# Kernel optimization log

Hardware: AMD Instinct MI355X
Metric: run time of the kernel (lower is better)

Reference implementation:

```python
import jax, jax.numpy as jnp
import numpy as np

L = 3            # max degree for L_in = L_edge = L_out = (0, 3)
B = 1024         # batch (number of edges)
C_IN = 256
C_OUT = 256
NUM_ORDERS = (L + 1) ** 2  # 16


def _build_structure(L):
    """Rebuild the coo_CG sparse structure: nonzeros sorted by (M_out, l1, l2),
    using the CG selection rule m1 + m2 = m for valid triangle triples."""
    triples = {}
    for l1 in range(L + 1):
        for l2 in range(L + 1):
            for l in range(abs(l1 - l2), min(L, l1 + l2) + 1):
                key = (l, l1, l2)
                if key not in triples:
                    triples[key] = len(triples)
    M1, M2, seg1, lind_g, seg2 = [], [], [], [], []
    g = 0
    for l in range(L + 1):
        for m in range(-l, l + 1):
            M = l * l + l + m  # flat order index of (l, m)
            for (lo, l1, l2) in sorted(triples.keys()):
                if lo != l:
                    continue
                cnt = 0
                for m1 in range(-l1, l1 + 1):
                    m2 = m - m1
                    if -l2 <= m2 <= l2:
                        M1.append(l1 * l1 + l1 + m1)
                        M2.append(l2 * l2 + l2 + m2)
                        seg1.append(g)
                        cnt += 1
                if cnt > 0:
                    lind_g.append(triples[(lo, l1, l2)])
                    seg2.append(M)
                    g += 1
    return (np.asarray(M1, np.int32), np.asarray(M2, np.int32),
            np.asarray(seg1, np.int32), np.asarray(lind_g, np.int32),
            np.asarray(seg2, np.int32), len(triples), g)


def setup_inputs() -> dict:
    key = jax.random.key(0)
    k1, k2, k3, k4 = jax.random.split(key, 4)
    M1, M2, seg1, l_ind, seg2, n_w, n_g = _build_structure(L)
    # expected: 478 nnz, 156 groups, 34 weights
    x = jax.random.normal(k1, (B, NUM_ORDERS, C_IN), jnp.float32)
    sh = jax.random.normal(k2, (B, NUM_ORDERS), jnp.float32)
    fan = np.sqrt(2.0 / (C_IN + C_OUT)).astype(np.float32)
    weight = jax.random.normal(k3, (n_w, C_IN, C_OUT), jnp.float32) * fan
    CG_vals = jax.random.normal(k4, (M1.shape[0],), jnp.float32) * 0.3
    return {
        'x': x, 'sh': sh, 'weight': weight, 'CG_vals': CG_vals,
        'M1': jnp.asarray(M1), 'M2': jnp.asarray(M2), 'seg1': jnp.asarray(seg1),
        'l_ind': jnp.asarray(l_ind), 'seg2': jnp.asarray(seg2),
        'num_orders_out': NUM_ORDERS,
    }


def reference(x, sh, weight, CG_vals, M1, M2, seg1, l_ind, seg2, num_orders_out):
    # x: (B, Mi, Ci); sh: (B, Me); weight: (num_weights, Ci, Co)
    Bn = x.shape[0]
    G = l_ind.shape[0]
    Ci = x.shape[-1]
    Co = weight.shape[-1]
    feat = x[:, M1, :]                                      # (B, nnz, Ci) gather on orders
    sh_g = sh[:, M2]                                        # (B, nnz)
    inter = (CG_vals[None, :] * sh_g)[..., None] * feat     # (B, nnz, Ci)
    inter = jnp.zeros((Bn, G, Ci), x.dtype).at[:, seg1, :].add(inter)   # segment over (M,l1,l2)
    w = weight[l_ind]                                       # (G, Ci, Co)
    ret = jnp.einsum('bgi,gio->bgo', inter, w)              # per-group matmul
    out = jnp.zeros((Bn, num_orders_out, Co), x.dtype).at[:, seg2, :].add(ret)  # segment over M
    return out
```

## Files before the change

### kernel.cpp

```cpp
#include <hip/hip_runtime.h>
#include <stdint.h>

#define B_SZ 1024
#define NO   16
#define CI   256
#define CO   256
#define BK   64
#define BM   32
#define LDA  72
#define MAXG 12
#define MAXE 48
#define WP   76

typedef unsigned short u16;
typedef __attribute__((ext_vector_type(8))) short short8;
typedef __attribute__((ext_vector_type(4))) float f32x4;
typedef __attribute__((ext_vector_type(4))) unsigned short u16x4;
typedef __attribute__((ext_vector_type(8))) unsigned short u16x8;

__device__ __forceinline__ u16 f2bf(float f) {
  union { float f; uint32_t u; } v; v.f = f;
  uint32_t u = v.u;
  return (u16)((u + 0x7FFFu + ((u >> 16) & 1u)) >> 16);
}
__device__ __forceinline__ float bf2f(u16 h) {
  union { float f; uint32_t u; } v; v.u = ((uint32_t)h) << 16; return v.f;
}

__device__ __forceinline__ f32x4 mfma_16x16x32_bf16(short8 a, short8 b, f32x4 c) {
  asm volatile("v_mfma_f32_16x16x32_bf16 %0, %1, %2, %0" : "+v"(c) : "v"(a), "v"(b));
  return c;
}

extern "C" __global__ void xconv_kernel(const float* __restrict__ x,
                                        u16* __restrict__ xbf, int n8) {
  int t = blockIdx.x * 256 + threadIdx.x;
  if (t >= n8) return;
  const float* s = x + (size_t)t * 8;
  float4 a = ((const float4*)s)[0];
  float4 b = ((const float4*)s)[1];
  u16x8 pk;
  pk[0] = f2bf(a.x); pk[1] = f2bf(a.y); pk[2] = f2bf(a.z); pk[3] = f2bf(a.w);
  pk[4] = f2bf(b.x); pk[5] = f2bf(b.y); pk[6] = f2bf(b.z); pk[7] = f2bf(b.w);
  *(u16x8*)(xbf + (size_t)t * 8) = pk;
}

extern "C" __global__ void wconv_kernel(const float* __restrict__ w,
                                        u16* __restrict__ wbf) {
  __shared__ u16 t_lds[64 * WP];
  const int tid = threadIdx.x;
  const int bid = blockIdx.x;
  const int wi = bid >> 4;
  const int i0 = ((bid >> 2) & 3) * 64;
  const int o0 = (bid & 3) * 64;
  const float* src = w + (size_t)wi * (CI * CO);
  u16* dst = wbf + (size_t)wi * (CI * CO);
#pragma unroll
  for (int p = 0; p < 4; ++p) {
    int idx = p * 256 + tid;
    int i = idx >> 4, oq = (idx & 15) * 4;
    float4 v = *(const float4*)(src + (size_t)(i0 + i) * CO + o0 + oq);
    t_lds[(oq + 0) * WP + i] = f2bf(v.x);
    t_lds[(oq + 1) * WP + i] = f2bf(v.y);
    t_lds[(oq + 2) * WP + i] = f2bf(v.z);
    t_lds[(oq + 3) * WP + i] = f2bf(v.w);
  }
  __syncthreads();
#pragma unroll
  for (int p = 0; p < 4; ++p) {
    int idx = p * 256 + tid;
    int o = idx >> 4, iq = (idx & 15) * 4;
    u16x4 v;
    v[0] = t_lds[o * WP + iq + 0]; v[1] = t_lds[o * WP + iq + 1];
    v[2] = t_lds[o * WP + iq + 2]; v[3] = t_lds[o * WP + iq + 3];
    *(u16x4*)(dst + (size_t)(o0 + o) * CI + i0 + iq) = v;
  }
}

extern "C" __global__ void __launch_bounds__(256, 4)
so3_main(const u16* __restrict__ xbf,
         const float* __restrict__ sh,
         const float* __restrict__ CG,
         const u16* __restrict__ wbf,
         const int* __restrict__ M1,
         const int* __restrict__ M2,
         const int* __restrict__ seg1,
         const int* __restrict__ lind,
         const int* __restrict__ seg2,
         float* __restrict__ out,
         int G, int nnz) {
  __shared__ u16 As[BM * LDA];
  __shared__ u16 Bs[128 * LDA];
  __shared__ float coefs[MAXE][BM];
  __shared__ int s_meta[4];
  __shared__ int s_estart[MAXG], s_eend[MAXG], s_wind[MAXG], s_m1[MAXE];

  const int tid = threadIdx.x;
  const int bid = blockIdx.x;
  const int b0  = (bid & 31) * BM;
  const int M   = (bid >> 5) & 15;
  const int co0 = (bid >> 9) * 128;

  if (tid == 0) { s_meta[0] = 1 << 30; s_meta[1] = 0; s_meta[2] = 1 << 30; s_meta[3] = 0; }
  if (tid < MAXG) { s_estart[tid] = 1 << 30; s_eend[tid] = 0; }
  __syncthreads();
  for (int g = tid; g < G; g += 256)
    if (seg2[g] == M) { atomicMin(&s_meta[0], g); atomicMax(&s_meta[1], g + 1); }
  __syncthreads();
  const int gstart = s_meta[0];
  const int ng = s_meta[1] - gstart;
  for (int e = tid; e < nnz; e += 256) {
    int g = seg1[e] - gstart;
    if (g >= 0 && g < ng) {
      atomicMin(&s_meta[2], e); atomicMax(&s_meta[3], e + 1);
      atomicMin(&s_estart[g], e); atomicMax(&s_eend[g], e + 1);
    }
  }
  __syncthreads();
  const int e0 = s_meta[2];
  const int ne = s_meta[3] - e0;
  for (int i = tid; i < ng; i += 256) s_wind[i] = lind[gstart + i];
  for (int i = tid; i < ne; i += 256) s_m1[i] = M1[e0 + i];
  for (int idx = tid; idx < ne * BM; idx += 256) {
    int el = idx / BM, r = idx & (BM - 1);
    int e = e0 + el;
    coefs[el][r] = CG[e] * sh[(size_t)(b0 + r) * NO + M2[e]];
  }
  __syncthreads();

  const int lane = tid & 63;
  const int wn = tid >> 6;
  const int lrow = lane & 15, lq = lane >> 4;
  const int ar = tid >> 3;
  const int ak = (tid & 7) * 8;

  f32x4 acc[2][2];
#pragma unroll
  for (int i = 0; i < 2; ++i)
#pragma unroll
    for (int j = 0; j < 2; ++j) acc[i][j] = (f32x4){0.f, 0.f, 0.f, 0.f};

  const int T = ng * 4;
  u16x8 breg[4];
  {
    const u16* wb = wbf + (size_t)s_wind[0] * (CI * CO) + (size_t)co0 * CI;
#pragma unroll
    for (int rr = 0; rr < 4; ++rr) {
      int idx = tid + rr * 256, o = idx >> 3, ic = (idx & 7) * 8;
      breg[rr] = *(const u16x8*)(wb + (size_t)o * CI + ic);
    }
  }

  for (int t = 0; t < T; ++t) {
    const int gl = t >> 2, kk = (t & 3) * BK;
    const int ea = s_estart[gl] - e0, eb = s_eend[gl] - e0;
    {
      const u16* xrow = xbf + (size_t)(b0 + ar) * (NO * CI) + kk + ak;
      float ax[8];
#pragma unroll
      for (int j = 0; j < 8; ++j) ax[j] = 0.f;
      for (int el = ea; el < eb; ++el) {
        float cf = coefs[el][ar];
        u16x8 xv = *(const u16x8*)(xrow + (size_t)s_m1[el] * CI);
#pragma unroll
        for (int j = 0; j < 8; ++j) ax[j] = fmaf(cf, bf2f(xv[j]), ax[j]);
      }
      u16x8 pk;
#pragma unroll
      for (int j = 0; j < 8; ++j) pk[j] = f2bf(ax[j]);
      *(u16x8*)&As[ar * LDA + ak] = pk;
    }
#pragma unroll
    for (int rr = 0; rr < 4; ++rr) {
      int idx = tid + rr * 256, o = idx >> 3, ic = (idx & 7) * 8;
      *(u16x8*)&Bs[o * LDA + ic] = breg[rr];
    }
    {
      int tn = (t + 1 < T) ? t + 1 : t;
      int gln = tn >> 2, kkn = (tn & 3) * BK;
      const u16* wbn = wbf + (size_t)s_wind[gln] * (CI * CO) + (size_t)co0 * CI + kkn;
#pragma unroll
      for (int rr = 0; rr < 4; ++rr) {
        int idx = tid + rr * 256, o = idx >> 3, ic = (idx & 7) * 8;
        breg[rr] = *(const u16x8*)(wbn + (size_t)o * CI + ic);
      }
    }
    __syncthreads();
#pragma unroll
    for (int ks = 0; ks < 2; ++ks) {
      short8 af[2], bfr[2];
#pragma unroll
      for (int mf = 0; mf < 2; ++mf)
        af[mf] = *(const short8*)&As[(mf * 16 + lrow) * LDA + ks * 32 + lq * 8];
#pragma unroll
      for (int nf = 0; nf < 2; ++nf)
        bfr[nf] = *(const short8*)&Bs[(wn * 32 + nf * 16 + lrow) * LDA + ks * 32 + lq * 8];
#pragma unroll
      for (int mf = 0; mf < 2; ++mf)
#pragma unroll
        for (int nf = 0; nf < 2; ++nf)
          acc[mf][nf] = mfma_16x16x32_bf16(af[mf], bfr[nf], acc[mf][nf]);
    }
    __syncthreads();
  }

#pragma unroll
  for (int mf = 0; mf < 2; ++mf) {
    int brow = b0 + mf * 16 + lq * 4;
#pragma unroll
    for (int nf = 0; nf < 2; ++nf) {
      int o = co0 + wn * 32 + nf * 16 + lrow;
#pragma unroll
      for (int rg = 0; rg < 4; ++rg)
        out[(size_t)(brow + rg) * (NO * CO) + (size_t)M * CO + o] = acc[mf][nf][rg];
    }
  }
}

extern "C" void kernel_launch(void* const* d_in, const int* in_sizes, int n_in,
                              void* d_out, int out_size, void* d_ws, size_t ws_size,
                              hipStream_t stream) {
  const float* x   = (const float*)d_in[0];
  const float* sh  = (const float*)d_in[1];
  const float* wgt = (const float*)d_in[2];
  const float* CG  = (const float*)d_in[3];
  const int* M1    = (const int*)d_in[4];
  const int* M2    = (const int*)d_in[5];
  const int* seg1  = (const int*)d_in[6];
  const int* lind  = (const int*)d_in[7];
  const int* seg2  = (const int*)d_in[8];
  float* out       = (float*)d_out;

  const int nnz = in_sizes[3];
  const int G   = in_sizes[7];
  const int n_w = in_sizes[2] / (CI * CO);

  u16* xbf = (u16*)d_ws;
  u16* wbf = (u16*)((char*)d_ws + (size_t)B_SZ * NO * CI * 2);

  int n8 = B_SZ * NO * CI / 8;
  xconv_kernel<<<dim3(n8 / 256), dim3(256), 0, stream>>>(x, xbf, n8);
  wconv_kernel<<<dim3(n_w * 16), dim3(256), 0, stream>>>(wgt, wbf);
  so3_main<<<dim3(1024), dim3(256), 0, stream>>>(xbf, sh, CG, wbf, M1, M2, seg1, lind, seg2,
                                                 out, G, nnz);
}
```

Before: 173.1 us.

## Load weight fragments directly to registers and double-buffer A tile

Removes the shared-memory staging of the weight tile: each wave now loads its own B fragments straight from global memory into registers in MFMA layout. The A tile is double-buffered in LDS so building the next A tile overlaps the MFMAs on the current one, with one barrier per step instead of two. It also uses the hardware packed bf16 conversion instruction instead of manual rounding. The cost is more registers for two B fragment sets and uncoalesced, less-shared global weight reads across waves. The loop steps by two and relies on T being even, which holds since T = ng*4.

After: 206.3 us. +19.2%, slower.

```diff
diff --git a/kernel.cpp b/kernel.cpp
--- a/kernel.cpp
+++ b/kernel.cpp
@@ -89,8 +89,7 @@
          const int* __restrict__ seg2,
          float* __restrict__ out,
          int G, int nnz) {
-  __shared__ u16 As[BM * LDA];
-  __shared__ u16 Bs[128 * LDA];
+  __shared__ u16 As[2][BM * LDA];
   __shared__ float coefs[MAXE][BM];
   __shared__ int s_meta[4];
   __shared__ int s_estart[MAXG], s_eend[MAXG], s_wind[MAXG], s_m1[MAXE];
@@ -141,67 +140,70 @@
     for (int j = 0; j < 2; ++j) acc[i][j] = (f32x4){0.f, 0.f, 0.f, 0.f};
 
   const int T = ng * 4;
-  u16x8 breg[4];
-  {
-    const u16* wb = wbf + (size_t)s_wind[0] * (CI * CO) + (size_t)co0 * CI;
-#pragma unroll
-    for (int rr = 0; rr < 4; ++rr) {
-      int idx = tid + rr * 256, o = idx >> 3, ic = (idx & 7) * 8;
-      breg[rr] = *(const u16x8*)(wb + (size_t)o * CI + ic);
-    }
-  }
-
-  for (int t = 0; t < T; ++t) {
-    const int gl = t >> 2, kk = (t & 3) * BK;
-    const int ea = s_estart[gl] - e0, eb = s_eend[gl] - e0;
-    {
-      const u16* xrow = xbf + (size_t)(b0 + ar) * (NO * CI) + kk + ak;
-      float ax[8];
-#pragma unroll
-      for (int j = 0; j < 8; ++j) ax[j] = 0.f;
-      for (int el = ea; el < eb; ++el) {
-        float cf = coefs[el][ar];
-        u16x8 xv = *(const u16x8*)(xrow + (size_t)s_m1[el] * CI);
-#pragma unroll
-        for (int j = 0; j < 8; ++j) ax[j] = fmaf(cf, bf2f(xv[j]), ax[j]);
-      }
-      u16x8 pk;
-#pragma unroll
-      for (int j = 0; j < 8; ++j) pk[j] = f2bf(ax[j]);
-      *(u16x8*)&As[ar * LDA + ak] = pk;
-    }
-#pragma unroll
-    for (int rr = 0; rr < 4; ++rr) {
-      int idx = tid + rr * 256, o = idx >> 3, ic = (idx & 7) * 8;
-      *(u16x8*)&Bs[o * LDA + ic] = breg[rr];
-    }
-    {
-      int tn = (t + 1 < T) ? t + 1 : t;
-      int gln = tn >> 2, kkn = (tn & 3) * BK;
-      const u16* wbn = wbf + (size_t)s_wind[gln] * (CI * CO) + (size_t)co0 * CI + kkn;
-#pragma unroll
-      for (int rr = 0; rr < 4; ++rr) {
-        int idx = tid + rr * 256, o = idx >> 3, ic = (idx & 7) * 8;
-        breg[rr] = *(const u16x8*)(wbn + (size_t)o * CI + ic);
-      }
-    }
+
+  auto loadB = [&](int tt, short8* dst) {
+    int gl = tt >> 2, kk = (tt & 3) * BK;
+    const u16* wb = wbf + (size_t)s_wind[gl] * (CI * CO)
+                  + (size_t)(co0 + wn * 32) * CI + kk;
+#pragma unroll
+    for (int nf = 0; nf < 2; ++nf)
+#pragma unroll
+      for (int ks = 0; ks < 2; ++ks)
+        dst[nf * 2 + ks] =
+            *(const short8*)(wb + (size_t)(nf * 16 + lrow) * CI + ks * 32 + lq * 8);
+  };
+
+  auto buildA = [&](int tt) {
+    int gl = tt >> 2, kk = (tt & 3) * BK;
+    int ea = s_estart[gl] - e0, eb = s_eend[gl] - e0;
+    const u16* xrow = xbf + (size_t)(b0 + ar) * (NO * CI) + kk + ak;
+    float ax[8];
+#pragma unroll
+    for (int j = 0; j < 8; ++j) ax[j] = 0.f;
+    for (int el = ea; el < eb; ++el) {
+      float cf = coefs[el][ar];
+      u16x8 xv = *(const u16x8*)(xrow + (size_t)s_m1[el] * CI);
+#pragma unroll
+      for (int j = 0; j < 8; ++j) ax[j] = fmaf(cf, bf2f(xv[j]), ax[j]);
+    }
+    uint32_t d0, d1, d2, d3;
+    asm("v_cvt_pk_bf16_f32 %0, %1, %2" : "=v"(d0) : "v"(ax[0]), "v"(ax[1]));
+    asm("v_cvt_pk_bf16_f32 %0, %1, %2" : "=v"(d1) : "v"(ax[2]), "v"(ax[3]));
+    asm("v_cvt_pk_bf16_f32 %0, %1, %2" : "=v"(d2) : "v"(ax[4]), "v"(ax[5]));
+    asm("v_cvt_pk_bf16_f32 %0, %1, %2" : "=v"(d3) : "v"(ax[6]), "v"(ax[7]));
+    union { u16x8 v; uint32_t d[4]; } u;
+    u.d[0] = d0; u.d[1] = d1; u.d[2] = d2; u.d[3] = d3;
+    *(u16x8*)&As[tt & 1][ar * LDA + ak] = u.v;
+  };
+
+  auto mmaPhase = [&](int tt, const short8* bc) {
+    const u16* Ab = As[tt & 1];
+#pragma unroll
+    for (int ks = 0; ks < 2; ++ks) {
+      short8 af[2];
+#pragma unroll
+      for (int mf = 0; mf < 2; ++mf)
+        af[mf] = *(const short8*)&Ab[(mf * 16 + lrow) * LDA + ks * 32 + lq * 8];
+#pragma unroll
+      for (int mf = 0; mf < 2; ++mf)
+#pragma unroll
+        for (int nf = 0; nf < 2; ++nf)
+          acc[mf][nf] = mfma_16x16x32_bf16(af[mf], bc[nf * 2 + ks], acc[mf][nf]);
+    }
+  };
+
+  short8 bA[4], bB[4];
+  buildA(0);
+  loadB(0, bA);
+  for (int t = 0; t < T; t += 2) {
     __syncthreads();
-#pragma unroll
-    for (int ks = 0; ks < 2; ++ks) {
-      short8 af[2], bfr[2];
-#pragma unroll
-      for (int mf = 0; mf < 2; ++mf)
-        af[mf] = *(const short8*)&As[(mf * 16 + lrow) * LDA + ks * 32 + lq * 8];
-#pragma unroll
-      for (int nf = 0; nf < 2; ++nf)
-        bfr[nf] = *(const short8*)&Bs[(wn * 32 + nf * 16 + lrow) * LDA + ks * 32 + lq * 8];
-#pragma unroll
-      for (int mf = 0; mf < 2; ++mf)
-#pragma unroll
-        for (int nf = 0; nf < 2; ++nf)
-          acc[mf][nf] = mfma_16x16x32_bf16(af[mf], bfr[nf], acc[mf][nf]);
-    }
+    loadB(t + 1, bB);
+    mmaPhase(t, bA);
+    buildA(t + 1);
     __syncthreads();
+    loadB(t + 2 < T ? t + 2 : t + 1, bA);
+    mmaPhase(t + 1, bB);
+    if (t + 2 < T) buildA(t + 2);
   }
 
 #pragma unroll
```

## Build full-K A tile once per group with batched, unrolled gather loads

Applied to the files above, without the earlier changes.

The A operand (CG-weighted sum of gathered x rows) is now built for the whole 256-wide K dimension once per group and kept in a larger LDS tile, instead of being rebuilt per 64-wide K step. The gather loop is unrolled over up to 8 entries, issuing paired loads to raise memory-level parallelism, and coefficients are stored as bf16 in LDS. This adds LDS use (which may lower occupancy) and more registers. It also silently caps each group at 8 nonzero entries, which holds for L=3 but is a structural assumption.

Measured after the change: 175.2 us. No clear change (+1.2%).

```diff
diff --git a/kernel.cpp b/kernel.cpp
--- a/kernel.cpp
+++ b/kernel.cpp
@@ -7,7 +7,8 @@
 #define CO   256
 #define BK   64
 #define BM   32
-#define LDA  72
+#define LDB  72
+#define LDAA 264
 #define MAXG 12
 #define MAXE 48
 #define WP   76
@@ -89,9 +90,9 @@
          const int* __restrict__ seg2,
          float* __restrict__ out,
          int G, int nnz) {
-  __shared__ u16 As[BM * LDA];
-  __shared__ u16 Bs[128 * LDA];
-  __shared__ float coefs[MAXE][BM];
+  __shared__ u16 As[BM * LDAA];
+  __shared__ u16 Bs[128 * LDB];
+  __shared__ u16 coefs[MAXE][BM];
   __shared__ int s_meta[4];
   __shared__ int s_estart[MAXG], s_eend[MAXG], s_wind[MAXG], s_m1[MAXE];
 
@@ -103,6 +104,7 @@
 
   if (tid == 0) { s_meta[0] = 1 << 30; s_meta[1] = 0; s_meta[2] = 1 << 30; s_meta[3] = 0; }
   if (tid < MAXG) { s_estart[tid] = 1 << 30; s_eend[tid] = 0; }
+  if (tid < MAXE) s_m1[tid] = 0;
   __syncthreads();
   for (int g = tid; g < G; g += 256)
     if (seg2[g] == M) { atomicMin(&s_meta[0], g); atomicMax(&s_meta[1], g + 1); }
@@ -124,7 +126,7 @@
   for (int idx = tid; idx < ne * BM; idx += 256) {
     int el = idx / BM, r = idx & (BM - 1);
     int e = e0 + el;
-    coefs[el][r] = CG[e] * sh[(size_t)(b0 + r) * NO + M2[e]];
+    coefs[el][r] = f2bf(CG[e] * sh[(size_t)(b0 + r) * NO + M2[e]]);
   }
   __syncthreads();
 
@@ -141,6 +143,50 @@
     for (int j = 0; j < 2; ++j) acc[i][j] = (f32x4){0.f, 0.f, 0.f, 0.f};
 
   const int T = ng * 4;
+
+  auto buildA = [&](int gl) {
+    const int ea = s_estart[gl] - e0;
+    const int cnt = (s_eend[gl] - e0) - ea;
+    const u16* xb = xbf + (size_t)(b0 + ar) * (NO * CI) + ak;
+    float cf[8]; int mo[8];
+    const int mo0 = s_m1[ea] * CI;
+#pragma unroll
+    for (int j = 0; j < 8; ++j) {
+      bool v = j < cnt;
+      cf[j] = v ? bf2f(coefs[ea + j][ar]) : 0.f;
+      mo[j] = v ? s_m1[ea + j] * CI : mo0;
+    }
+    float ax[4][8];
+#pragma unroll
+    for (int q = 0; q < 4; ++q)
+#pragma unroll
+      for (int j = 0; j < 8; ++j) ax[q][j] = 0.f;
+#pragma unroll
+    for (int p = 0; p < 4; ++p) {
+      if (2 * p < cnt) {
+        u16x8 vX[4], vY[4];
+#pragma unroll
+        for (int q = 0; q < 4; ++q) vX[q] = *(const u16x8*)(xb + mo[2 * p] + q * 64);
+#pragma unroll
+        for (int q = 0; q < 4; ++q) vY[q] = *(const u16x8*)(xb + mo[2 * p + 1] + q * 64);
+        const float c0 = cf[2 * p], c1 = cf[2 * p + 1];
+#pragma unroll
+        for (int q = 0; q < 4; ++q)
+#pragma unroll
+          for (int j = 0; j < 8; ++j)
+            ax[q][j] = fmaf(c1, bf2f((u16)vY[q][j]),
+                       fmaf(c0, bf2f((u16)vX[q][j]), ax[q][j]));
+      }
+    }
+#pragma unroll
+    for (int q = 0; q < 4; ++q) {
+      u16x8 pk;
+#pragma unroll
+      for (int j = 0; j < 8; ++j) pk[j] = f2bf(ax[q][j]);
+      *(u16x8*)&As[ar * LDAA + q * 64 + ak] = pk;
+    }
+  };
+
   u16x8 breg[4];
   {
     const u16* wb = wbf + (size_t)s_wind[0] * (CI * CO) + (size_t)co0 * CI;
@@ -152,28 +198,12 @@
   }
 
   for (int t = 0; t < T; ++t) {
-    const int gl = t >> 2, kk = (t & 3) * BK;
-    const int ea = s_estart[gl] - e0, eb = s_eend[gl] - e0;
-    {
-      const u16* xrow = xbf + (size_t)(b0 + ar) * (NO * CI) + kk + ak;
-      float ax[8];
-#pragma unroll
-      for (int j = 0; j < 8; ++j) ax[j] = 0.f;
-      for (int el = ea; el < eb; ++el) {
-        float cf = coefs[el][ar];
-        u16x8 xv = *(const u16x8*)(xrow + (size_t)s_m1[el] * CI);
-#pragma unroll
-        for (int j = 0; j < 8; ++j) ax[j] = fmaf(cf, bf2f(xv[j]), ax[j]);
-      }
-      u16x8 pk;
-#pragma unroll
-      for (int j = 0; j < 8; ++j) pk[j] = f2bf(ax[j]);
-      *(u16x8*)&As[ar * LDA + ak] = pk;
-    }
+    const int gl = t >> 2, kk = t & 3;
+    if (kk == 0) buildA(gl);
 #pragma unroll
     for (int rr = 0; rr < 4; ++rr) {
       int idx = tid + rr * 256, o = idx >> 3, ic = (idx & 7) * 8;
-      *(u16x8*)&Bs[o * LDA + ic] = breg[rr];
+      *(u16x8*)&Bs[o * LDB + ic] = breg[rr];
     }
     {
       int tn = (t + 1 < T) ? t + 1 : t;
@@ -191,10 +221,10 @@
       short8 af[2], bfr[2];
 #pragma unroll
       for (int mf = 0; mf < 2; ++mf)
-        af[mf] = *(const short8*)&As[(mf * 16 + lrow) * LDA + ks * 32 + lq * 8];
+        af[mf] = *(const short8*)&As[(mf * 16 + lrow) * LDAA + kk * 64 + ks * 32 + lq * 8];
 #pragma unroll
       for (int nf = 0; nf < 2; ++nf)
-        bfr[nf] = *(const short8*)&Bs[(wn * 32 + nf * 16 + lrow) * LDA + ks * 32 + lq * 8];
+        bfr[nf] = *(const short8*)&Bs[(wn * 32 + nf * 16 + lrow) * LDB + ks * 32 + lq * 8];
 #pragma unroll
       for (int mf = 0; mf < 2; ++mf)
 #pragma unroll
```
